# Kernel optimization log

Hardware: AMD Instinct MI355X
Metric: run time of the kernel (lower is better)

The kernel has to match this reference:

```python
import jax, jax.numpy as jnp
import numpy as np
from jax.scipy.special import erfc

# ---- static config (matches init_kwargs) ----
N_ATOMS = 16384
NUM_BATCH = 32
N_PAIRS = 1_048_576
KMAX = 8
CUTOFF = 10.0
ON_CUT = 0.25 * CUTOFF   # 2.5
OFF_CUT = 0.75 * CUTOFF  # 7.5
ALPHA = 4.0 / CUTOFF + 0.001
ALPHA2 = ALPHA * ALPHA
TWO_PI = 2.0 * np.pi
ONE_OVER_SQRTPI = 1.0 / np.sqrt(np.pi)
EPS = 1e-8


def _make_kmul():
    r = np.arange(-KMAX, KMAX + 1)
    kx, ky, kz = np.meshgrid(r, r, r, indexing='ij')
    k = np.stack([kx, ky, kz], axis=-1).reshape(-1, 3).astype(np.float32)
    k2 = np.sum(k * k, axis=-1)
    k = k[(k2 > 0) & (k2 <= KMAX ** 2)]  # exclude k=0, spherical cutoff
    return k  # [K, 3]


def setup_inputs() -> dict:
    key = jax.random.key(0)
    ks = jax.random.split(key, 6)
    Qa = 0.5 * jax.random.normal(ks[0], (N_ATOMS,), dtype=jnp.float32)
    rij = 0.5 + 9.5 * jax.random.uniform(ks[1], (N_PAIRS,), dtype=jnp.float32)
    R = 20.0 * jax.random.uniform(ks[2], (N_ATOMS, 3), dtype=jnp.float32)
    boxlen = 18.0 + 4.0 * jax.random.uniform(ks[3], (NUM_BATCH, 3), dtype=jnp.float32)
    cell = boxlen[:, :, None] * jnp.eye(3, dtype=jnp.float32)[None]  # diagonal boxes [B,3,3]
    idx_i = jnp.sort(jax.random.randint(ks[4], (N_PAIRS,), 0, N_ATOMS)).astype(jnp.int32)
    idx_j = jax.random.randint(ks[5], (N_PAIRS,), 0, N_ATOMS).astype(jnp.int32)
    batch_seg = jnp.repeat(jnp.arange(NUM_BATCH, dtype=jnp.int32), N_ATOMS // NUM_BATCH)
    kmul = jnp.asarray(_make_kmul())
    return {"Qa": Qa, "rij": rij, "R": R, "cell": cell, "kmul": kmul,
            "idx_i": idx_i, "idx_j": idx_j, "batch_seg": batch_seg}


def _switch_component(x):
    x_safe = jnp.where(x <= 0, jnp.ones_like(x), x)
    return jnp.where(x <= 0, jnp.zeros_like(x), jnp.exp(-1.0 / x_safe))


def _switch_function(r):
    # smooth C-inf switch: 1 for r<=ON_CUT, 0 for r>=OFF_CUT
    x = (r - ON_CUT) / (OFF_CUT - ON_CUT)
    fp = _switch_component(x)
    fm = _switch_component(1.0 - x)
    return jnp.where(x <= 0, jnp.ones_like(x),
                     jnp.where(x >= 1, jnp.zeros_like(x), fm / (fp + fm)))


def _real_space(Qa, rij, idx_i, idx_j):
    fac = Qa[idx_i] * Qa[idx_j]                    # gather per pair
    f = _switch_function(rij)
    coulomb = 1.0 / rij
    damped = 1.0 / jnp.sqrt(rij * rij + 1.0)
    pw = fac * (f * damped + (1.0 - f) * coulomb) * erfc(ALPHA * rij)
    return jax.ops.segment_sum(pw, idx_i, num_segments=N_ATOMS)  # [N]


def _reciprocal_space(q, R, cell, kmul, batch_seg):
    box_length = jnp.diagonal(cell, axis1=-2, axis2=-1)            # [B,3]
    k = TWO_PI * kmul[None, :, :] / box_length[:, None, :]         # [B,K,3]
    k2 = jnp.sum(k * k, axis=-1)                                   # [B,K]
    qg = jnp.exp(-0.25 * k2 / ALPHA2) / k2                         # [B,K]
    dot = jnp.sum(k[batch_seg] * R[:, None, :], axis=-1)           # [N,K]
    qcos = q[:, None] * jnp.cos(dot)                               # [N,K]
    qsin = q[:, None] * jnp.sin(dot)
    q_real = jax.ops.segment_sum(qcos, batch_seg, num_segments=NUM_BATCH)  # [B,K]
    q_imag = jax.ops.segment_sum(qsin, batch_seg, num_segments=NUM_BATCH)
    qf = q_real * q_real + q_imag * q_imag
    e_recip_b = TWO_PI / jnp.prod(box_length, axis=1) * jnp.sum(qf * qg, axis=-1)  # [B]
    q2 = q * q
    e_self = ALPHA * ONE_OVER_SQRTPI * q2                          # [N]
    w = q2 + EPS
    wnorm = jax.ops.segment_sum(w, batch_seg, num_segments=NUM_BATCH)
    w = w / wnorm[batch_seg]
    return w * e_recip_b[batch_seg] - e_self                       # [N]


def reference(Qa, rij, R, cell, kmul, idx_i, idx_j, batch_seg):
    e_real = _real_space(Qa, rij, idx_i, idx_j)
    e_recip = _reciprocal_space(Qa, R, cell, kmul, batch_seg)
    return e_real + e_recip  # per-atom electrostatic energy [N]
```

## Files before the change

### kernel.cpp

```cpp
#include <hip/hip_runtime.h>

#define N_ATOMS 16384
#define NUM_BATCH 32
#define N_PAIRS 1048576
#define ATOMS_PER_BATCH 512

#define C_TWO_PI 6.28318530717958647692f
#define C_ALPHA 0.401f
#define C_ALPHA2 0.160801f
#define C_SELF 0.22624002f
#define C_EPS 1e-8f

__device__ __forceinline__ float switch_fn(float r) {
    float x = (r - 2.5f) * 0.2f;
    if (x <= 0.0f) return 1.0f;
    if (x >= 1.0f) return 0.0f;
    float fp = __expf(-1.0f / x);
    float fm = __expf(-1.0f / (1.0f - x));
    return fm / (fp + fm);
}

#define ASPLIT 4

__global__ __launch_bounds__(256) void recip_kernel(
    const float* __restrict__ Qa, const float* __restrict__ R,
    const float* __restrict__ cell, const float* __restrict__ kmul,
    float* __restrict__ partials, int K, int nchunk) {
    __shared__ float4 at[ATOMS_PER_BATCH];
    __shared__ float pr[ASPLIT][64];
    __shared__ float pi_[ASPLIT][64];

    int b  = blockIdx.y;
    int tx = threadIdx.x;
    int ty = threadIdx.y;
    int flat = ty * 64 + tx;

    float Lx = cell[b * 9 + 0], Ly = cell[b * 9 + 4], Lz = cell[b * 9 + 8];
    float iLx = 1.0f / Lx, iLy = 1.0f / Ly, iLz = 1.0f / Lz;

    int abase = b * ATOMS_PER_BATCH;
    for (int a = flat; a < ATOMS_PER_BATCH; a += 256) {
        int n = abase + a;
        at[a] = make_float4(R[3 * n + 0] * iLx, R[3 * n + 1] * iLy,
                            R[3 * n + 2] * iLz, Qa[n]);
    }
    __syncthreads();

    int K2 = K >> 1;
    int kk = K2 + blockIdx.x * 64 + tx;
    bool valid = kk < K;
    int kki = valid ? kk : K2;
    float mx = kmul[3 * kki + 0];
    float my = kmul[3 * kki + 1];
    float mz = kmul[3 * kki + 2];

    float cr = 0.0f, ci = 0.0f;
    int a0 = ty * (ATOMS_PER_BATCH / ASPLIT);
#pragma unroll 4
    for (int a = a0; a < a0 + (ATOMS_PER_BATCH / ASPLIT); ++a) {
        float4 v = at[a];
        float dr = mx * v.x + my * v.y + mz * v.z;
        float ang = C_TWO_PI * (dr - rintf(dr));
        cr = fmaf(v.w, __cosf(ang), cr);
        ci = fmaf(v.w, __sinf(ang), ci);
    }

    if (ty > 0) { pr[ty][tx] = cr; pi_[ty][tx] = ci; }
    __syncthreads();
    if (ty == 0) {
#pragma unroll
        for (int s = 1; s < ASPLIT; ++s) { cr += pr[s][tx]; ci += pi_[s][tx]; }
        float kx = C_TWO_PI * mx * iLx;
        float ky = C_TWO_PI * my * iLy;
        float kz = C_TWO_PI * mz * iLz;
        float k2 = kx * kx + ky * ky + kz * kz;
        float qg = __expf(-0.25f * k2 / C_ALPHA2) / k2;
        float contrib = valid ? 2.0f * (cr * cr + ci * ci) * qg : 0.0f;
#pragma unroll
        for (int off = 32; off > 0; off >>= 1)
            contrib += __shfl_down(contrib, off);
        if (tx == 0)
            partials[b * nchunk + blockIdx.x] =
                (C_TWO_PI / (Lx * Ly * Lz)) * contrib;
    }
}

#define LPA 4
#define SUBS 8
#define APB (ATOMS_PER_BATCH / SUBS)

__global__ __launch_bounds__(256) void final_kernel(
    const float* __restrict__ Qa, const float* __restrict__ rij,
    const int* __restrict__ idx_i, const int* __restrict__ idx_j,
    const float* __restrict__ partials, int nchunk,
    float* __restrict__ out) {
    int b   = blockIdx.x >> 3;
    int sub = blockIdx.x & 7;
    int tid = threadIdx.x;
    int abase = b * ATOMS_PER_BATCH;

    float q0 = Qa[abase + tid];
    float q1 = Qa[abase + 256 + tid];
    float s = fmaf(q0, q0, C_EPS) + fmaf(q1, q1, C_EPS);
#pragma unroll
    for (int off = 32; off > 0; off >>= 1) s += __shfl_down(s, off);
    __shared__ float red[4];
    __shared__ float bc[2];
    if ((tid & 63) == 0) red[tid >> 6] = s;
    __syncthreads();
    if (tid == 0) {
        float w = red[0] + red[1] + red[2] + red[3];
        float er = 0.0f;
        for (int c = 0; c < nchunk; ++c) er += partials[b * nchunk + c];
        bc[0] = w; bc[1] = er;
    }
    __syncthreads();
    float wnorm   = bc[0];
    float e_recip = bc[1];

    int atom = abase + sub * APB + (tid >> 2);
    int g = tid & 3;

    int lo = 0, hi = N_PAIRS;
    while (lo < hi) { int mid = (lo + hi) >> 1; if (idx_i[mid] < atom) lo = mid + 1; else hi = mid; }
    int start = lo;
    lo = 0; hi = N_PAIRS;
    int key = atom + 1;
    while (lo < hi) { int mid = (lo + hi) >> 1; if (idx_i[mid] < key) lo = mid + 1; else hi = mid; }
    int end = lo;

    float qi = Qa[atom];
    float acc = 0.0f;
    for (int p = start + g; p < end; p += LPA) {
        float r = rij[p];
        float f = switch_fn(r);
        float coul   = __builtin_amdgcn_rcpf(r);
        float damped = __builtin_amdgcn_rsqf(fmaf(r, r, 1.0f));
        float qj = Qa[idx_j[p]];
        acc = fmaf(qj, (f * damped + (1.0f - f) * coul) * erfcf(C_ALPHA * r), acc);
    }
    acc *= qi;
    acc += __shfl_xor(acc, 1);
    acc += __shfl_xor(acc, 2);

    if (g == 0) {
        float q2 = qi * qi;
        float w = (q2 + C_EPS) / wnorm;
        out[atom] = acc + w * e_recip - C_SELF * q2;
    }
}

extern "C" void kernel_launch(void* const* d_in, const int* in_sizes, int n_in,
                              void* d_out, int out_size, void* d_ws, size_t ws_size,
                              hipStream_t stream) {
    const float* Qa   = (const float*)d_in[0];
    const float* rij  = (const float*)d_in[1];
    const float* R    = (const float*)d_in[2];
    const float* cell = (const float*)d_in[3];
    const float* kmul = (const float*)d_in[4];
    const int* idx_i  = (const int*)d_in[5];
    const int* idx_j  = (const int*)d_in[6];
    float* out = (float*)d_out;

    int K = in_sizes[4] / 3;
    int K2 = K / 2;
    int nchunk = (K2 + 63) / 64;

    float* partials = (float*)d_ws;

    dim3 rblock(64, ASPLIT);
    dim3 rgrid(nchunk, NUM_BATCH);
    recip_kernel<<<rgrid, rblock, 0, stream>>>(Qa, R, cell, kmul, partials, K, nchunk);

    final_kernel<<<NUM_BATCH * SUBS, 256, 0, stream>>>(
        Qa, rij, idx_i, idx_j, partials, nchunk, out);
}
```

Baseline: 110.4 us.

## Parallelize final kernel over pair ranges with wave-ballot search and LDS atomics

Replaces the per-atom scalar binary searches with two wave-cooperative 64-way ballot searches that find the block's pair range. The block then streams that contiguous range using int4/float4 vector loads and accumulates per-atom sums in shared memory with run-length merged atomics. The work splits into 16 sub-blocks per batch instead of 8, and the partials reduction becomes a wave shuffle. This is meant to cut the serialized, divergent binary-search latency and to improve coalescing and load balance. The cost is shared-memory atomics and a Qa[idx_i] gather per pair.

```diff
diff --git a/kernel.cpp b/kernel.cpp
--- a/kernel.cpp
+++ b/kernel.cpp
@@ -85,68 +85,112 @@
     }
 }
 
-#define LPA 4
-#define SUBS 8
-#define APB (ATOMS_PER_BATCH / SUBS)
+__device__ __forceinline__ int lower_bound64(const int* __restrict__ arr, int key) {
+    int lane = threadIdx.x & 63;
+    int lo = 0, size = N_PAIRS;
+    while (size > 64) {
+        int chunk = (size + 63) >> 6;
+        int pos = lo + (lane + 1) * chunk;
+        int v = (pos < lo + size) ? arr[pos] : 0x7fffffff;
+        unsigned long long m = __ballot(v < key);
+        int cnt = __popcll(m);
+        int nlo = lo + cnt * chunk;
+        size = min(chunk, lo + size - nlo);
+        lo = nlo;
+    }
+    int pos = lo + lane;
+    int v = (lane < size) ? arr[pos] : 0x7fffffff;
+    unsigned long long m = __ballot(v < key);
+    return lo + __popcll(m);
+}
+
+#define SUBS 16
+#define NA (ATOMS_PER_BATCH / SUBS)
 
 __global__ __launch_bounds__(256) void final_kernel(
     const float* __restrict__ Qa, const float* __restrict__ rij,
     const int* __restrict__ idx_i, const int* __restrict__ idx_j,
     const float* __restrict__ partials, int nchunk,
     float* __restrict__ out) {
-    int b   = blockIdx.x >> 3;
-    int sub = blockIdx.x & 7;
-    int tid = threadIdx.x;
+    __shared__ float accs[NA];
+    __shared__ float red[4];
+    __shared__ float er_s;
+    __shared__ int   se[2];
+
+    int b    = blockIdx.x >> 4;
+    int sub  = blockIdx.x & 15;
+    int tid  = threadIdx.x;
+    int wave = tid >> 6;
     int abase = b * ATOMS_PER_BATCH;
+    int A0 = abase + sub * NA;
+
+    if (tid < NA) accs[tid] = 0.0f;
 
     float q0 = Qa[abase + tid];
     float q1 = Qa[abase + 256 + tid];
     float s = fmaf(q0, q0, C_EPS) + fmaf(q1, q1, C_EPS);
 #pragma unroll
     for (int off = 32; off > 0; off >>= 1) s += __shfl_down(s, off);
-    __shared__ float red[4];
-    __shared__ float bc[2];
-    if ((tid & 63) == 0) red[tid >> 6] = s;
-    __syncthreads();
-    if (tid == 0) {
-        float w = red[0] + red[1] + red[2] + red[3];
-        float er = 0.0f;
-        for (int c = 0; c < nchunk; ++c) er += partials[b * nchunk + c];
-        bc[0] = w; bc[1] = er;
-    }
-    __syncthreads();
-    float wnorm   = bc[0];
-    float e_recip = bc[1];
-
-    int atom = abase + sub * APB + (tid >> 2);
-    int g = tid & 3;
-
-    int lo = 0, hi = N_PAIRS;
-    while (lo < hi) { int mid = (lo + hi) >> 1; if (idx_i[mid] < atom) lo = mid + 1; else hi = mid; }
-    int start = lo;
-    lo = 0; hi = N_PAIRS;
-    int key = atom + 1;
-    while (lo < hi) { int mid = (lo + hi) >> 1; if (idx_i[mid] < key) lo = mid + 1; else hi = mid; }
-    int end = lo;
-
-    float qi = Qa[atom];
-    float acc = 0.0f;
-    for (int p = start + g; p < end; p += LPA) {
-        float r = rij[p];
-        float f = switch_fn(r);
-        float coul   = __builtin_amdgcn_rcpf(r);
-        float damped = __builtin_amdgcn_rsqf(fmaf(r, r, 1.0f));
-        float qj = Qa[idx_j[p]];
-        acc = fmaf(qj, (f * damped + (1.0f - f) * coul) * erfcf(C_ALPHA * r), acc);
-    }
-    acc *= qi;
-    acc += __shfl_xor(acc, 1);
-    acc += __shfl_xor(acc, 2);
-
-    if (g == 0) {
-        float q2 = qi * qi;
+    if ((tid & 63) == 0) red[wave] = s;
+
+    if (wave == 0) {
+        int r = lower_bound64(idx_i, A0);
+        if ((tid & 63) == 0) se[0] = r;
+    } else if (wave == 1) {
+        int r = lower_bound64(idx_i, A0 + NA);
+        if ((tid & 63) == 0) se[1] = r;
+    } else if (wave == 2) {
+        int c = tid - 128;
+        float er = (c < nchunk) ? partials[b * nchunk + c] : 0.0f;
+#pragma unroll
+        for (int off = 32; off > 0; off >>= 1) er += __shfl_down(er, off);
+        if (c == 0) er_s = er;
+    }
+    __syncthreads();
+
+    float wnorm   = red[0] + red[1] + red[2] + red[3];
+    float e_recip = er_s;
+    int start = se[0], end = se[1];
+
+    int s4 = start >> 2;
+    int e4 = (end + 3) >> 2;
+    for (int g4 = s4 + tid; g4 < e4; g4 += 256) {
+        int4   ii = ((const int4*)idx_i)[g4];
+        int4   jj = ((const int4*)idx_j)[g4];
+        float4 rr = ((const float4*)rij)[g4];
+        int   is[4] = {ii.x, ii.y, ii.z, ii.w};
+        int   js[4] = {jj.x, jj.y, jj.z, jj.w};
+        float rs[4] = {rr.x, rr.y, rr.z, rr.w};
+        int cur = -1;
+        float acc = 0.0f;
+        int p0 = g4 << 2;
+#pragma unroll
+        for (int u = 0; u < 4; ++u) {
+            int p = p0 + u;
+            if (p < start || p >= end) continue;
+            float r = rs[u];
+            float f = switch_fn(r);
+            float coul   = __builtin_amdgcn_rcpf(r);
+            float damped = __builtin_amdgcn_rsqf(fmaf(r, r, 1.0f));
+            float pw = Qa[is[u]] * Qa[js[u]] *
+                       (f * damped + (1.0f - f) * coul) * erfcf(C_ALPHA * r);
+            if (is[u] != cur) {
+                if (cur >= 0) atomicAdd(&accs[cur - A0], acc);
+                cur = is[u];
+                acc = 0.0f;
+            }
+            acc += pw;
+        }
+        if (cur >= 0) atomicAdd(&accs[cur - A0], acc);
+    }
+    __syncthreads();
+
+    if (tid < NA) {
+        int atom = A0 + tid;
+        float q = Qa[atom];
+        float q2 = q * q;
         float w = (q2 + C_EPS) / wnorm;
-        out[atom] = acc + w * e_recip - C_SELF * q2;
+        out[atom] = accs[tid] + w * e_recip - C_SELF * q2;
     }
 }
 
```

New measurement: 95.58 us. 1.15x faster.
